# Optimization experiments

Measured on AMD Instinct MI355X. Metric: run time of the kernel, lower is better.

Reference implementation:

```python
import jax, jax.numpy as jnp
import numpy as np

NEG_SLOPE = 0.01  # torch LeakyReLU default


def _conv1x1_lrelu(x, W, b):
    # x: [B,C,H,W], W: [C,C] (out,in), b: [C]
    y = jnp.einsum('oc,bchw->bohw', W, x) + b[None, :, None, None]
    return jax.nn.leaky_relu(y, NEG_SLOPE)


def setup_inputs() -> dict:
    key = jax.random.key(0)
    B, C, H, Wd = 4, 64, 64, 64
    ks = jax.random.split(key, 9)
    scale = 1.0 / np.sqrt(C)  # torch Conv2d default init range ~ U(-1/sqrt(fan_in), ...)
    inp = {'x': jax.random.normal(ks[0], (B, C, H, Wd), dtype=jnp.float32)}
    for i in range(4):
        inp[f'W{i+1}'] = jax.random.uniform(ks[1 + 2 * i], (C, C), minval=-scale, maxval=scale, dtype=jnp.float32)
        inp[f'b{i+1}'] = jax.random.uniform(ks[2 + 2 * i], (C,), minval=-scale, maxval=scale, dtype=jnp.float32)
    return inp


def reference(x, W1, b1, W2, b2, W3, b3, W4, b4):
    B, C, H, Wd = x.shape
    N = H * Wd
    x1 = _conv1x1_lrelu(x, W1, b1).reshape(B, C, N)
    x2 = _conv1x1_lrelu(x, W2, b2).reshape(B, C, N)
    x3 = _conv1x1_lrelu(x, W3, b3).reshape(B, C, N)
    # raw (unscaled) attention scores, softmax over dim=1 (the 'n' axis)
    a = jnp.einsum('bcn,bcm->bnm', x1, x2)
    a = jax.nn.softmax(a, axis=1)
    out = jnp.einsum('bcn,bnm->bcm', x3, a).reshape(B, C, H, Wd)
    out = _conv1x1_lrelu(out, W4, b4) + x
    return out
```

## Files before the change

### kernel.cpp

```cpp
#include <hip/hip_runtime.h>
#include <hip/hip_bf16.h>
#include <math.h>

using f32x4 = __attribute__((ext_vector_type(4))) float;
using s16x8 = __attribute__((ext_vector_type(8))) short;
using s16x4 = __attribute__((ext_vector_type(4))) short;

#define LOG2E 1.44269504f

__device__ __forceinline__ unsigned short f2bf(float f) {
  unsigned int u = __builtin_bit_cast(unsigned int, f);
  u += 0x7FFFu + ((u >> 16) & 1u);
  return (unsigned short)(u >> 16);
}
__device__ __forceinline__ float lrelu(float v) { return v > 0.f ? v : 0.01f * v; }

__device__ __forceinline__ unsigned packbf(float lo, float hi) {
  return __builtin_amdgcn_perm(__builtin_bit_cast(unsigned, hi),
                               __builtin_bit_cast(unsigned, lo), 0x07060302u);
}
__device__ __forceinline__ float redsum_lh(float x) {
  x += __shfl_xor(x, 16);
  x += __shfl_xor(x, 32);
  return x;
}
__device__ __forceinline__ void xswap(unsigned& A, unsigned& B, int X) {
  const int lane = (int)(threadIdx.x & 63);
  unsigned sel = (lane & X) ? A : B;
  unsigned ex = (unsigned)__shfl_xor((int)sel, X);
  A = (lane & X) ? ex : A;
  B = (lane & X) ? B : ex;
}

#define GLL16(src, dst)                                                        \
  __builtin_amdgcn_global_load_lds(                                            \
      (const __attribute__((address_space(1))) void*)(src),                    \
      (__attribute__((address_space(3))) void*)(dst), 16, 0, 0)

#define K1_W 8192
#define K1_X3 32768
#define K1_SM 41984

__global__ __launch_bounds__(256) void k1_conv3(
    const float* __restrict__ x,
    const float* __restrict__ W1, const float* __restrict__ b1,
    const float* __restrict__ W2, const float* __restrict__ b2,
    const float* __restrict__ W3, const float* __restrict__ b3,
    unsigned short* __restrict__ x1t, unsigned short* __restrict__ x2t,
    unsigned short* __restrict__ x3) {
  __shared__ __align__(16) char SM[K1_SM];
  char* smB = (char*)SM;
  const int t = threadIdx.x;
  const int b = blockIdx.x >> 6;
  const int n0 = (blockIdx.x & 63) << 6;
  const int lane = t & 63, wave = t >> 6;
  const int l15 = lane & 15, lh = lane >> 4;
  const int swz = (l15 & 7) << 4;

  const float* Ws[3] = {W1, W2, W3};
  char* Wb = smB + K1_W;
#pragma unroll
  for (int w = 0; w < 3; ++w)
#pragma unroll
    for (int it = 0; it < 4; ++it) {
      const int c = t >> 2, k4 = (t & 3) * 16 + it * 4;
      const float4 wv = *(const float4*)(Ws[w] + c * 64 + k4);
      char* dst = Wb + w * 8192 + c * 128 + ((k4 * 2) ^ ((c & 7) << 4));
      *(unsigned*)dst = packbf(wv.x, wv.y);
      *(unsigned*)(dst + 4) = packbf(wv.z, wv.w);
    }
  char* XT = smB;
#pragma unroll
  for (int it = 0; it < 4; ++it) {
    const int k = (t >> 4) + it * 16, n4 = (t & 15) * 4;
    const float4 xv = *(const float4*)(x + ((size_t)b * 64 + k) * 4096 + n0 + n4);
#pragma unroll
    for (int j = 0; j < 4; ++j) {
      const int n = n4 + j;
      *(unsigned short*)(XT + n * 128 + ((k * 2) ^ ((n & 7) << 4))) =
          f2bf(((const float*)&xv)[j]);
    }
  }
  __syncthreads();

  s16x8 bf0, bf1;
  {
    const char* xr = XT + (wave * 16 + l15) * 128;
    bf0 = *(const s16x8*)(xr + ((lh * 16) ^ swz));
    bf1 = *(const s16x8*)(xr + ((lh * 16 + 64) ^ swz));
  }
  char* sX3 = smB + K1_X3;
#pragma unroll
  for (int w = 0; w < 3; ++w) {
    const float* bb = (w == 0) ? b1 : (w == 1) ? b2 : b3;
#pragma unroll
    for (int ci = 0; ci < 4; ++ci) {
      f32x4 acc = *(const f32x4*)(bb + ci * 16 + lh * 4);
      const char* wr = Wb + w * 8192 + (ci * 16 + l15) * 128;
      const s16x8 af0 = *(const s16x8*)(wr + ((lh * 16) ^ swz));
      const s16x8 af1 = *(const s16x8*)(wr + ((lh * 16 + 64) ^ swz));
      acc = __builtin_amdgcn_mfma_f32_16x16x32_bf16(af0, bf0, acc, 0, 0, 0);
      acc = __builtin_amdgcn_mfma_f32_16x16x32_bf16(af1, bf1, acc, 0, 0, 0);
      float v[4];
#pragma unroll
      for (int r = 0; r < 4; ++r) v[r] = lrelu(acc[r]);
      if (w == 1)
#pragma unroll
        for (int r = 0; r < 4; ++r) v[r] *= LOG2E;
      if (w < 2) {
        unsigned pk[2] = {packbf(v[0], v[1]), packbf(v[2], v[3])};
        unsigned short* base = (w ? x2t : x1t);
        unsigned short* dst =
            base + ((size_t)b * 4096 + n0 + wave * 16 + l15) * 64 + ci * 16 + lh * 4;
        *(uint2*)dst = *(const uint2*)pk;
      } else {
#pragma unroll
        for (int r = 0; r < 4; ++r)
          *(unsigned short*)(sX3 + (ci * 16 + lh * 4 + r) * 144 +
                             (wave * 16 + l15) * 2) = f2bf(v[r]);
      }
    }
  }
  __syncthreads();
  {
    const int c2 = t >> 2, q = t & 3;
    const s16x8 v0 = *(const s16x8*)(sX3 + c2 * 144 + q * 32);
    const s16x8 v1 = *(const s16x8*)(sX3 + c2 * 144 + q * 32 + 16);
    unsigned short* dst = x3 + ((size_t)b * 64 + c2) * 4096 + n0 + q * 16;
    *(s16x8*)dst = v0;
    *(s16x8*)(dst + 8) = v1;
  }
}

#define KOFF 0
#define VOFF 65536
#define W4OFF 131072
#define SLOFF 148480
#define SMSZ 150528

__global__ __launch_bounds__(1024) void k2_attn_fused(
    const unsigned short* __restrict__ x1t,
    const unsigned short* __restrict__ x2t,
    const unsigned short* __restrict__ x3,
    const float* __restrict__ W4, const float* __restrict__ b4,
    const float* __restrict__ x, float* __restrict__ out) {
  __shared__ __align__(16) char SM[SMSZ];
  char* smB = (char*)SM;

  const int t = threadIdx.x;
  const int wave = t >> 6, lane = t & 63;
  const int l15 = lane & 15, lh = lane >> 4;
  const int msub = wave & 1, split = wave >> 1;
  const int b = blockIdx.x >> 6;
  const int m0 = (blockIdx.x & 63) << 6;
  const int nb = split * 512;

  const char* x1B = (const char*)(x1t + (size_t)b * 4096 * 64);
  const char* x3B = (const char*)(x3 + (size_t)b * 64 * 4096);
  const unsigned short* x2b = x2t + (size_t)b * 4096 * 64;

  {
    float* Wt4 = (float*)(smB + W4OFF);
    for (int e = t; e < 4096; e += 1024) Wt4[(e & 63) * 68 + (e >> 6)] = W4[e];
  }

  int kSrcOff[2], vSrcOff[2];
  char *kDst[2], *vDst[2];
#pragma unroll
  for (int i = 0; i < 2; ++i) {
    const int o = msub * 2048 + i * 1024 + lane * 16;
    {
      const int n = o >> 7, cb = (o & 127) ^ ((n & 7) << 4);
      kSrcOff[i] = n * 128 + cb;
      kDst[i] = smB + KOFF + split * 4096 + msub * 2048 + i * 1024;
    }
    {
      const int ch = o >> 7, rem = (o & 127) ^ ((ch & 7) << 4);
      vSrcOff[i] = (ch * 2 + (rem >> 6)) * 8192 + (rem & 63);
      vDst[i] = smB + VOFF + split * 4096 + msub * 2048 + i * 1024;
    }
  }

  s16x8 qf[2][2];
#pragma unroll
  for (int q2 = 0; q2 < 2; ++q2) {
    const unsigned short* qp = x2b + (size_t)(m0 + msub * 32 + q2 * 16 + l15) * 64 + lh * 8;
    qf[q2][0] = *(const s16x8*)qp;
    qf[q2][1] = *(const s16x8*)(qp + 32);
  }

  f32x4 O[2][4];
#pragma unroll
  for (int q2 = 0; q2 < 2; ++q2)
#pragma unroll
    for (int s = 0; s < 4; ++s) O[q2][s] = (f32x4){0.f, 0.f, 0.f, 0.f};
  float l_part[2] = {0.f, 0.f};

  const int swzK = (l15 & 7) << 4;
  const int swzV = ((l15 >> 1) & 7) << 4;

#pragma unroll
  for (int i = 0; i < 2; ++i) {
    GLL16(x1B + (size_t)nb * 128 + kSrcOff[i], kDst[i]);
    GLL16(x3B + (size_t)nb * 2 + vSrcOff[i], vDst[i]);
  }
  __syncthreads();

  for (int j = 0; j < 16; ++j) {
    const int p = j & 1;
    if (j < 15) {
      const int nstep = nb + (j + 1) * 32;
      const int po = (p ^ 1) * 32768;
#pragma unroll
      for (int i = 0; i < 2; ++i) {
        GLL16(x1B + (size_t)nstep * 128 + kSrcOff[i], kDst[i] + po);
        GLL16(x3B + (size_t)nstep * 2 + vSrcOff[i], vDst[i] + po);
      }
    }
    s16x8 kf[2][2], vf[4];
#pragma unroll
    for (int s2 = 0; s2 < 2; ++s2) {
      const char* kp = smB + KOFF + p * 32768 + split * 4096 + (s2 * 16 + l15) * 128;
      kf[s2][0] = *(const s16x8*)(kp + ((lh * 16) ^ swzK));
      kf[s2][1] = *(const s16x8*)(kp + ((lh * 16 + 64) ^ swzK));
    }
    const char* vp = smB + VOFF + p * 32768 + split * 4096;
#pragma unroll
    for (int s = 0; s < 4; ++s) {
      const int c = s * 16 + l15;
      vf[s] = *(const s16x8*)(vp + (c >> 1) * 128 + (((c & 1) * 64 + lh * 16) ^ swzV));
    }
    f32x4 S[2][2];
#pragma unroll
    for (int q2 = 0; q2 < 2; ++q2)
#pragma unroll
      for (int s2 = 0; s2 < 2; ++s2) {
        f32x4 z = {0.f, 0.f, 0.f, 0.f};
        z = __builtin_amdgcn_mfma_f32_16x16x32_bf16(kf[s2][0], qf[q2][0], z, 0, 0, 0);
        S[q2][s2] = __builtin_amdgcn_mfma_f32_16x16x32_bf16(kf[s2][1], qf[q2][1], z, 0, 0, 0);
      }
    s16x8 pf[2];
#pragma unroll
    for (int q2 = 0; q2 < 2; ++q2) {
      float pr[2][4];
      float ts = 0.f;
#pragma unroll
      for (int s2 = 0; s2 < 2; ++s2)
#pragma unroll
        for (int r = 0; r < 4; ++r) {
          pr[s2][r] = __builtin_amdgcn_exp2f(S[q2][s2][r]);
          ts += pr[s2][r];
        }
      l_part[q2] += ts;
      unsigned u00 = packbf(pr[0][0], pr[0][1]), u01 = packbf(pr[0][2], pr[0][3]);
      unsigned u10 = packbf(pr[1][0], pr[1][1]), u11 = packbf(pr[1][2], pr[1][3]);
      xswap(u00, u10, 32); xswap(u01, u11, 32);
      xswap(u00, u10, 16); xswap(u01, u11, 16);
      int4 w = {(int)u00, (int)u01, (int)u10, (int)u11};
      pf[q2] = __builtin_bit_cast(s16x8, w);
    }
#pragma unroll
    for (int q2 = 0; q2 < 2; ++q2)
#pragma unroll
      for (int s = 0; s < 4; ++s)
        O[q2][s] = __builtin_amdgcn_mfma_f32_16x16x32_bf16(vf[s], pf[q2], O[q2][s], 0, 0, 0);
    __syncthreads();
  }

  float* cOf = (float*)smB;
  float* sLf = (float*)(smB + SLOFF);
#pragma unroll
  for (int q2 = 0; q2 < 2; ++q2) {
    const float l = redsum_lh(l_part[q2]);
    const int m32 = q2 * 16 + l15;
    if (lh == 0) sLf[wave * 32 + m32] = l;
#pragma unroll
    for (int s = 0; s < 4; ++s)
      *(f32x4*)(cOf + wave * 2048 + m32 * 64 + s * 16 + lh * 4) = O[q2][s];
  }
  __syncthreads();

  const int mloc = t & 63, cq = t >> 6;
  const int msub2 = mloc >> 5, m32b = mloc & 31;
  float den = 0.f, num[4] = {0.f, 0.f, 0.f, 0.f};
#pragma unroll
  for (int s2 = 0; s2 < 8; ++s2) {
    const int w = msub2 + 2 * s2;
    den += sLf[w * 32 + m32b];
    const f32x4 cv = *(const f32x4*)(cOf + w * 2048 + m32b * 64 + cq * 4);
#pragma unroll
    for (int jj = 0; jj < 4; ++jj) num[jj] += cv[jj];
  }
  const float inv = 1.f / den;
  __syncthreads();
  float* attnS = (float*)smB;
#pragma unroll
  for (int jj = 0; jj < 4; ++jj) attnS[(cq * 4 + jj) * 65 + mloc] = num[jj] * inv;
  __syncthreads();

  const float* Wt4 = (const float*)(smB + W4OFF);
  const int co0 = cq * 4;
  float acc[4];
#pragma unroll
  for (int ci = 0; ci < 4; ++ci) acc[ci] = b4[co0 + ci];
  for (int k = 0; k < 64; ++k) {
    const float a = attnS[k * 65 + mloc];
    const float4 wv = *(const float4*)&Wt4[k * 68 + co0];
#pragma unroll
    for (int ci = 0; ci < 4; ++ci)
      acc[ci] = __builtin_fmaf(((const float*)&wv)[ci], a, acc[ci]);
  }
#pragma unroll
  for (int ci = 0; ci < 4; ++ci) {
    const size_t idx = ((size_t)b * 64 + co0 + ci) * 4096 + m0 + mloc;
    out[idx] = lrelu(acc[ci]) + x[idx];
  }
}

extern "C" void kernel_launch(void* const* d_in, const int* in_sizes, int n_in,
                              void* d_out, int out_size, void* d_ws, size_t ws_size,
                              hipStream_t stream) {
  const float* x = (const float*)d_in[0];
  const float* W1 = (const float*)d_in[1];
  const float* b1 = (const float*)d_in[2];
  const float* W2 = (const float*)d_in[3];
  const float* b2 = (const float*)d_in[4];
  const float* W3 = (const float*)d_in[5];
  const float* b3 = (const float*)d_in[6];
  const float* W4 = (const float*)d_in[7];
  const float* b4 = (const float*)d_in[8];
  float* out = (float*)d_out;

  const size_t planes = (size_t)4 * 4096 * 64;
  unsigned short* x1t = (unsigned short*)d_ws;
  unsigned short* x2t = x1t + planes;
  unsigned short* x3 = x2t + planes;

  hipLaunchKernelGGL(k1_conv3, dim3(256), dim3(256), 0, stream,
                     x, W1, b1, W2, b2, W3, b3, x1t, x2t, x3);
  hipLaunchKernelGGL(k2_attn_fused, dim3(256), dim3(1024), 0, stream,
                     x1t, x2t, x3, W4, b4, x, out);
}
```

Measured before the change: 50.99 us.

## Store V in MFMA-fragment tile layout to drop P-fragment lane shuffles

The conv kernel now writes x3 in a pre-permuted, swizzled tile layout, 32 positions by 64 channels per tile. The attention kernel can then load V fragments whose k-ordering matches the softmax P registers directly, so the four xswap cross-lane shuffles per q-row per step go away. It also remaps block IDs so consecutive launched blocks span different batches and query tiles. The cost is a scalar gather with short LDS reads when k1 stores its output, and a tighter coupling of the layout to the MFMA fragment ordering.

Result: faster. 43.96 us (-13.8%).

```diff
diff --git a/kernel.cpp b/kernel.cpp
--- a/kernel.cpp
+++ b/kernel.cpp
@@ -23,13 +23,6 @@
   x += __shfl_xor(x, 16);
   x += __shfl_xor(x, 32);
   return x;
-}
-__device__ __forceinline__ void xswap(unsigned& A, unsigned& B, int X) {
-  const int lane = (int)(threadIdx.x & 63);
-  unsigned sel = (lane & X) ? A : B;
-  unsigned ex = (unsigned)__shfl_xor((int)sel, X);
-  A = (lane & X) ? ex : A;
-  B = (lane & X) ? B : ex;
 }
 
 #define GLL16(src, dst)                                                        \
@@ -47,7 +40,7 @@
     const float* __restrict__ W2, const float* __restrict__ b2,
     const float* __restrict__ W3, const float* __restrict__ b3,
     unsigned short* __restrict__ x1t, unsigned short* __restrict__ x2t,
-    unsigned short* __restrict__ x3) {
+    unsigned short* __restrict__ x3f) {
   __shared__ __align__(16) char SM[K1_SM];
   char* smB = (char*)SM;
   const int t = threadIdx.x;
@@ -123,12 +116,23 @@
   }
   __syncthreads();
   {
-    const int c2 = t >> 2, q = t & 3;
-    const s16x8 v0 = *(const s16x8*)(sX3 + c2 * 144 + q * 32);
-    const s16x8 v1 = *(const s16x8*)(sX3 + c2 * 144 + q * 32 + 16);
-    unsigned short* dst = x3 + ((size_t)b * 64 + c2) * 4096 + n0 + q * 16;
-    *(s16x8*)dst = v0;
-    *(s16x8*)(dst + 8) = v1;
+    char* x3fB = (char*)x3f;
+#pragma unroll
+    for (int u = 0; u < 2; ++u) {
+      const int e = t * 2 + u;
+      const int p8 = e & 7, r = (e >> 3) & 31, tl = e >> 8;
+      const int cid = p8 ^ (r & 7);
+      const int c = r + 32 * (cid >> 2);
+      const int h = cid & 3;
+      s16x8 v;
+#pragma unroll
+      for (int i = 0; i < 4; ++i) {
+        v[i] = *(const short*)(sX3 + c * 144 + (tl * 32 + h * 4 + i) * 2);
+        v[i + 4] = *(const short*)(sX3 + c * 144 + (tl * 32 + 16 + h * 4 + i) * 2);
+      }
+      const size_t tile = (size_t)b * 128 + (n0 >> 5) + tl;
+      *(s16x8*)(x3fB + ((tile * 32 + r) * 8 + p8) * 16) = v;
+    }
   }
 }
 
@@ -141,7 +145,7 @@
 __global__ __launch_bounds__(1024) void k2_attn_fused(
     const unsigned short* __restrict__ x1t,
     const unsigned short* __restrict__ x2t,
-    const unsigned short* __restrict__ x3,
+    const unsigned short* __restrict__ x3f,
     const float* __restrict__ W4, const float* __restrict__ b4,
     const float* __restrict__ x, float* __restrict__ out) {
   __shared__ __align__(16) char SM[SMSZ];
@@ -151,12 +155,13 @@
   const int wave = t >> 6, lane = t & 63;
   const int l15 = lane & 15, lh = lane >> 4;
   const int msub = wave & 1, split = wave >> 1;
-  const int b = blockIdx.x >> 6;
-  const int m0 = (blockIdx.x & 63) << 6;
+  const int bid = ((blockIdx.x & 7) << 5) | (blockIdx.x >> 3);
+  const int b = bid >> 6;
+  const int m0 = (bid & 63) << 6;
   const int nb = split * 512;
 
   const char* x1B = (const char*)(x1t + (size_t)b * 4096 * 64);
-  const char* x3B = (const char*)(x3 + (size_t)b * 64 * 4096);
+  const char* x3B = (const char*)x3f + (size_t)b * 524288;
   const unsigned short* x2b = x2t + (size_t)b * 4096 * 64;
 
   {
@@ -174,11 +179,8 @@
       kSrcOff[i] = n * 128 + cb;
       kDst[i] = smB + KOFF + split * 4096 + msub * 2048 + i * 1024;
     }
-    {
-      const int ch = o >> 7, rem = (o & 127) ^ ((ch & 7) << 4);
-      vSrcOff[i] = (ch * 2 + (rem >> 6)) * 8192 + (rem & 63);
-      vDst[i] = smB + VOFF + split * 4096 + msub * 2048 + i * 1024;
-    }
+    vSrcOff[i] = o;
+    vDst[i] = smB + VOFF + split * 4096 + msub * 2048 + i * 1024;
   }
 
   s16x8 qf[2][2];
@@ -197,12 +199,11 @@
   float l_part[2] = {0.f, 0.f};
 
   const int swzK = (l15 & 7) << 4;
-  const int swzV = ((l15 >> 1) & 7) << 4;
 
 #pragma unroll
   for (int i = 0; i < 2; ++i) {
     GLL16(x1B + (size_t)nb * 128 + kSrcOff[i], kDst[i]);
-    GLL16(x3B + (size_t)nb * 2 + vSrcOff[i], vDst[i]);
+    GLL16(x3B + (size_t)(nb >> 5) * 4096 + vSrcOff[i], vDst[i]);
   }
   __syncthreads();
 
@@ -214,7 +215,7 @@
 #pragma unroll
       for (int i = 0; i < 2; ++i) {
         GLL16(x1B + (size_t)nstep * 128 + kSrcOff[i], kDst[i] + po);
-        GLL16(x3B + (size_t)nstep * 2 + vSrcOff[i], vDst[i] + po);
+        GLL16(x3B + (size_t)(nstep >> 5) * 4096 + vSrcOff[i], vDst[i] + po);
       }
     }
     s16x8 kf[2][2], vf[4];
@@ -226,10 +227,9 @@
     }
     const char* vp = smB + VOFF + p * 32768 + split * 4096;
 #pragma unroll
-    for (int s = 0; s < 4; ++s) {
-      const int c = s * 16 + l15;
-      vf[s] = *(const s16x8*)(vp + (c >> 1) * 128 + (((c & 1) * 64 + lh * 16) ^ swzV));
-    }
+    for (int s = 0; s < 4; ++s)
+      vf[s] = *(const s16x8*)(vp + ((s & 1) * 16 + l15) * 128 +
+                              (((s >> 1) * 64 + lh * 16) ^ swzK));
     f32x4 S[2][2];
 #pragma unroll
     for (int q2 = 0; q2 < 2; ++q2)
@@ -252,12 +252,9 @@
           ts += pr[s2][r];
         }
       l_part[q2] += ts;
-      unsigned u00 = packbf(pr[0][0], pr[0][1]), u01 = packbf(pr[0][2], pr[0][3]);
-      unsigned u10 = packbf(pr[1][0], pr[1][1]), u11 = packbf(pr[1][2], pr[1][3]);
-      xswap(u00, u10, 32); xswap(u01, u11, 32);
-      xswap(u00, u10, 16); xswap(u01, u11, 16);
-      int4 w = {(int)u00, (int)u01, (int)u10, (int)u11};
-      pf[q2] = __builtin_bit_cast(s16x8, w);
+      int4 pw = {(int)packbf(pr[0][0], pr[0][1]), (int)packbf(pr[0][2], pr[0][3]),
+                 (int)packbf(pr[1][0], pr[1][1]), (int)packbf(pr[1][2], pr[1][3])};
+      pf[q2] = __builtin_bit_cast(s16x8, pw);
     }
 #pragma unroll
     for (int q2 = 0; q2 < 2; ++q2)
@@ -334,10 +331,10 @@
   const size_t planes = (size_t)4 * 4096 * 64;
   unsigned short* x1t = (unsigned short*)d_ws;
   unsigned short* x2t = x1t + planes;
-  unsigned short* x3 = x2t + planes;
+  unsigned short* x3f = x2t + planes;
 
   hipLaunchKernelGGL(k1_conv3, dim3(256), dim3(256), 0, stream,
-                     x, W1, b1, W2, b2, W3, b3, x1t, x2t, x3);
+                     x, W1, b1, W2, b2, W3, b3, x1t, x2t, x3f);
   hipLaunchKernelGGL(k2_attn_fused, dim3(256), dim3(1024), 0, stream,
-                     x1t, x2t, x3, W4, b4, x, out);
-}
+                     x1t, x2t, x3f, W4, b4, x, out);
+}
```
